# Kernel optimization log

Measured on AMD Instinct MI355X. Metric: run time of the kernel, lower is better.

Reference implementation:

```python
import jax, jax.numpy as jnp
import numpy as np

D_MODEL = 768
N_HEADS = 12
D_K = D_MODEL // N_HEADS
NEG_INF = -1e10


def setup_inputs() -> dict:
    key = jax.random.key(0)
    ks = jax.random.split(key, 12)
    B, S = 2, 4096
    scale = 1.0 / np.sqrt(D_MODEL)
    inp = {
        "q": jax.random.normal(ks[0], (B, S, D_MODEL), jnp.float32),
        "k": jax.random.normal(ks[1], (B, S, D_MODEL), jnp.float32),
        "v": jax.random.normal(ks[2], (B, S, D_MODEL), jnp.float32),
        "mask": jnp.ones((B, S), jnp.int32),
        "Wq": jax.random.normal(ks[3], (D_MODEL, D_MODEL), jnp.float32) * scale,
        "bq": jnp.zeros((D_MODEL,), jnp.float32),
        "Wk": jax.random.normal(ks[4], (D_MODEL, D_MODEL), jnp.float32) * scale,
        "bk": jnp.zeros((D_MODEL,), jnp.float32),
        "Wv": jax.random.normal(ks[5], (D_MODEL, D_MODEL), jnp.float32) * scale,
        "bv": jnp.zeros((D_MODEL,), jnp.float32),
        "Wo": jax.random.normal(ks[6], (D_MODEL, D_MODEL), jnp.float32) * scale,
        "bo": jnp.zeros((D_MODEL,), jnp.float32),
    }
    return inp


def reference(q, k, v, mask, Wq, bq, Wk, bk, Wv, bv, Wo, bo):
    B, Sq, _ = q.shape
    Sk = k.shape[1]
    # linear projections (flax Linear: x @ kernel + bias)
    query = q @ Wq + bq
    key_ = k @ Wk + bk
    value = v @ Wv + bv
    # split heads: [B, H, S, d_k]
    query = query.reshape(B, Sq, N_HEADS, D_K).transpose(0, 2, 1, 3)
    key_ = key_.reshape(B, Sk, N_HEADS, D_K).transpose(0, 2, 1, 3)
    value = value.reshape(B, Sk, N_HEADS, D_K).transpose(0, 2, 1, 3)
    # scores [B, H, Sq, Sk]
    scores = jnp.einsum('bhqd,bhkd->bhqk', query, key_) / jnp.sqrt(
        jnp.asarray(D_K, query.dtype))
    m = mask[:, None, None, :]  # 2D mask -> [B,1,1,Sk]
    scores = jnp.where(m == 0, NEG_INF, scores)
    attn = jax.nn.softmax(scores, axis=-1)
    # dropout deterministic (is_training=False): identity
    x = jnp.einsum('bhqk,bhkd->bhqd', attn, value)
    x = x.transpose(0, 2, 1, 3).reshape(B, Sq, D_MODEL)
    return x @ Wo + bo
```

## Files before the change

kernel.cpp:

```cpp
#include <hip/hip_runtime.h>

typedef __attribute__((ext_vector_type(8))) short short8;
typedef __attribute__((ext_vector_type(4))) float floatx4;
typedef __attribute__((ext_vector_type(16))) float floatx16;
typedef unsigned short ushort_t;

#define S_LEN 4096
#define NH 12
#define DK 64
#define DM 768
#define BQ 128
#define LOG2E 1.4426950408889634f

static __device__ __forceinline__ unsigned short f2bf(float f) {
    unsigned int u = __float_as_uint(f);
    u += 0x7FFFu + ((u >> 16) & 1u);
    return (unsigned short)(u >> 16);
}
static __device__ __forceinline__ unsigned pack2(float a, float b) {
    return (unsigned)f2bf(a) | ((unsigned)f2bf(b) << 16);
}
static __device__ __forceinline__ unsigned pack2f(float a, float b) {
    unsigned au = __float_as_uint(a) + 0x8000u;
    unsigned bu = __float_as_uint(b) + 0x8000u;
    return (bu & 0xFFFF0000u) | (au >> 16);
}
static __device__ __forceinline__ void gld_lds16(const void* g, void* l) {
    __builtin_amdgcn_global_load_lds(
        (__attribute__((address_space(1))) void*)g,
        (__attribute__((address_space(3))) void*)l, 16, 0, 0);
}

__global__ __launch_bounds__(256)
void wtrans_kernel(const float* __restrict__ W0, const float* __restrict__ W1,
                   const float* __restrict__ W2, const float* __restrict__ W3,
                   ushort_t* __restrict__ T0, ushort_t* __restrict__ T1,
                   ushort_t* __restrict__ T2, ushort_t* __restrict__ T3) {
    __shared__ float tile[32][33];
    const int z = blockIdx.z;
    const float* W = (z == 0) ? W0 : (z == 1) ? W1 : (z == 2) ? W2 : W3;
    ushort_t* T = (z == 0) ? T0 : (z == 1) ? T1 : (z == 2) ? T2 : T3;
    const int bx = blockIdx.x, by = blockIdx.y;
    const int tx = threadIdx.x, ty = threadIdx.y;
    #pragma unroll
    for (int j = 0; j < 32; j += 8)
        tile[ty + j][tx] = W[(size_t)(by * 32 + ty + j) * DM + bx * 32 + tx];
    __syncthreads();
    #pragma unroll
    for (int j = 0; j < 32; j += 8)
        T[(size_t)(bx * 32 + ty + j) * DM + by * 32 + tx] = f2bf(tile[tx][ty + j]);
}

__global__ __launch_bounds__(256)
void cvt_kernel(const float* __restrict__ A0, const float* __restrict__ A1,
                const float* __restrict__ A2, ushort_t* __restrict__ O0,
                ushort_t* __restrict__ O1, ushort_t* __restrict__ O2) {
    const int z = blockIdx.y;
    const float* A = (z == 0) ? A0 : (z == 1) ? A1 : A2;
    ushort_t* O = (z == 0) ? O0 : (z == 1) ? O1 : O2;
    const size_t i = ((size_t)blockIdx.x * 256 + threadIdx.x) * 8;
    const float4 f0 = *(const float4*)(A + i);
    const float4 f1 = *(const float4*)(A + i + 4);
    uint4 o;
    o.x = pack2(f0.x, f0.y);
    o.y = pack2(f0.z, f0.w);
    o.z = pack2(f1.x, f1.y);
    o.w = pack2(f1.z, f1.w);
    *(uint4*)(O + i) = o;
}

__global__ __launch_bounds__(256)
void vtrans_kernel(const ushort_t* __restrict__ Vn, ushort_t* __restrict__ Vt) {
    __shared__ ushort_t tl[64 * 72];
    const int s0 = blockIdx.x * 64;
    const size_t bh = blockIdx.y;
    const int t = threadIdx.x;
    {
        const int r = t >> 2, c0 = (t & 3) * 16;
        const uint4* src = (const uint4*)(Vn + (bh * S_LEN + s0 + r) * DK + c0);
        uint4 a0 = src[0], a1 = src[1];
        uint4* dst = (uint4*)&tl[r * 72 + c0];
        dst[0] = a0;
        dst[1] = a1;
    }
    __syncthreads();
    {
        const int d = t >> 2, c0 = (t & 3) * 16;
        alignas(16) ushort_t tmp[16];
        #pragma unroll
        for (int j = 0; j < 16; ++j) tmp[j] = tl[(c0 + j) * 72 + d];
        uint4* dst = (uint4*)(Vt + (bh * DK + d) * S_LEN + s0 + c0);
        dst[0] = *(const uint4*)&tmp[0];
        dst[1] = *(const uint4*)&tmp[8];
    }
}

struct GemmArgs {
    const ushort_t* A[3];
    const ushort_t* Wt[3];
    const float* bias[3];
    void* C[3];
    float scale[3];
};

template <int MODE>
__global__ __launch_bounds__(256, 3)
void gemm_kernel(GemmArgs args) {
    __shared__ ushort_t As[128 * 32];
    __shared__ ushort_t Bs[128 * 32];
    const int z = blockIdx.z;
    const ushort_t* A = args.A[z];
    const ushort_t* Wt = args.Wt[z];
    const float* bias = args.bias[z];
    void* Carg = args.C[z];
    const float scale = args.scale[z];

    const int m0 = blockIdx.x * 128;
    const int n0 = blockIdx.y * 128;
    const int t = threadIdx.x;
    const int w = t >> 6, lane = t & 63, l15 = lane & 15, quad = lane >> 4;
    const int rowoff = (w >> 1) * 64, coloff = (w & 1) * 64;
    const int srow = w * 16 + (lane >> 2);
    const int scol = (lane & 3) * 8;

    floatx4 acc[4][4];
    #pragma unroll
    for (int i = 0; i < 4; ++i)
        #pragma unroll
        for (int j = 0; j < 4; ++j) acc[i][j] = (floatx4){0.f, 0.f, 0.f, 0.f};

    for (int kt = 0; kt < DM; kt += 32) {
        __syncthreads();
        #pragma unroll
        for (int j = 0; j < 2; ++j) {
            const int r = j * 64 + srow;
            gld_lds16(A + (size_t)(m0 + r) * DM + kt + scol, &As[r * 32 + scol]);
            gld_lds16(Wt + (size_t)(n0 + r) * DM + kt + scol, &Bs[r * 32 + scol]);
        }
        __asm__ __volatile__("s_waitcnt vmcnt(0)" ::: "memory");
        __syncthreads();
        short8 af[4], bfr[4];
        #pragma unroll
        for (int i = 0; i < 4; ++i)
            af[i] = *(const short8*)&As[(rowoff + 16 * i + l15) * 32 + quad * 8];
        #pragma unroll
        for (int j = 0; j < 4; ++j)
            bfr[j] = *(const short8*)&Bs[(coloff + 16 * j + l15) * 32 + quad * 8];
        #pragma unroll
        for (int i = 0; i < 4; ++i)
            #pragma unroll
            for (int j = 0; j < 4; ++j)
                acc[i][j] = __builtin_amdgcn_mfma_f32_16x16x32_bf16(af[i], bfr[j], acc[i][j], 0, 0, 0);
    }

    #pragma unroll
    for (int i = 0; i < 4; ++i) {
        #pragma unroll
        for (int j = 0; j < 4; ++j) {
            #pragma unroll
            for (int reg = 0; reg < 4; ++reg) {
                const int m = m0 + rowoff + 16 * i + quad * 4 + reg;
                const int n = n0 + coloff + 16 * j + l15;
                const float v2 = (acc[i][j][reg] + bias[n]) * scale;
                if (MODE == 0) {
                    ushort_t* Out = (ushort_t*)Carg;
                    const int b = m >> 12, s = m & 4095, h = n >> 6, d = n & 63;
                    Out[((size_t)((b * NH + h) * S_LEN + s)) * DK + d] = f2bf(v2);
                } else {
                    float* Out = (float*)Carg;
                    Out[(size_t)m * DM + n] = v2;
                }
            }
        }
    }
}

__global__ __launch_bounds__(256, 3)
void attn_kernel(const ushort_t* __restrict__ Q, const ushort_t* __restrict__ K,
                 const ushort_t* __restrict__ VT, const int* __restrict__ mask,
                 ushort_t* __restrict__ X) {
    __shared__ ushort_t Qs[BQ * DK];
    __shared__ ushort_t Ks0[64 * DK], Ks1[64 * DK];
    __shared__ ushort_t Vs0[64 * DK], Vs1[64 * DK];

    const int id = blockIdx.x;
    const int per = id >> 3;
    const int bh = (id & 7) * 3 + (per >> 5);
    const int qb = per & 31;
    const int b = bh / NH, h = bh - b * NH;
    const size_t bho = (size_t)bh * S_LEN;
    const ushort_t* Vbase = VT + (size_t)bh * DK * S_LEN;
    const int t = threadIdx.x;
    const int w = t >> 6, lane = t & 63, l31 = lane & 31, half = lane >> 5;
    const int q0 = qb * BQ;
    const int swl = l31 & 7;
    const int frow8 = lane >> 3;
    const int fcc = lane & 7;

    auto fillK = [&](int kv0, ushort_t* Kb) {
        #pragma unroll
        for (int j = 0; j < 2; ++j) {
            const int r = (w * 2 + j) * 8 + frow8;
            const int c8 = fcc ^ (r & 7);
            gld_lds16(K + (bho + kv0 + r) * DK + c8 * 8, &Kb[r * DK + fcc * 8]);
        }
    };
    auto fillV = [&](int kv0, ushort_t* Vb) {
        #pragma unroll
        for (int j = 0; j < 2; ++j) {
            const int r = (w * 2 + j) * 8 + frow8;
            const int c8 = fcc ^ (r & 7);
            gld_lds16(Vbase + (size_t)r * S_LEN + kv0 + c8 * 8, &Vb[r * DK + fcc * 8]);
        }
    };

    fillK(0, Ks0);
    fillV(0, Vs0);
    #pragma unroll
    for (int j = 0; j < 4; ++j) {
        const int r = (w * 4 + j) * 8 + frow8;
        const int c8 = fcc ^ (r & 7);
        gld_lds16(Q + (bho + q0 + r) * DK + c8 * 8, &Qs[r * DK + fcc * 8]);
    }
    int ok = 1;
    {
        const int* mrow = mask + (size_t)b * S_LEN + t * 16;
        #pragma unroll
        for (int i = 0; i < 4; ++i) {
            const int4 mm = *(const int4*)(mrow + i * 4);
            ok &= (mm.x != 0) & (mm.y != 0) & (mm.z != 0) & (mm.w != 0);
        }
    }
    const int allones = __syncthreads_and(ok);

    short8 qf[4];
    #pragma unroll
    for (int ks = 0; ks < 4; ++ks) {
        const int c8 = ks * 2 + half;
        qf[ks] = *(const short8*)&Qs[(w * 32 + l31) * DK + ((c8 ^ swl) << 3)];
    }
    ushort_t* Ps = &Qs[(w * 32) * DK];

    floatx16 o[2];
    #pragma unroll
    for (int dt = 0; dt < 2; ++dt)
        #pragma unroll
        for (int r = 0; r < 16; ++r) o[dt][r] = 0.f;
    float l_r = 0.f;

    auto body = [&](int it, const ushort_t* Kc, const ushort_t* Vc,
                    ushort_t* Kn, ushort_t* Vn) {
        __syncthreads();
        if (it + 1 < S_LEN / 64) {
            fillK((it + 1) * 64, Kn);
            fillV((it + 1) * 64, Vn);
        }
        unsigned long long mb = ~0ULL;
        if (!allones) {
            const int mv = mask[(size_t)b * S_LEN + it * 64 + lane];
            mb = __ballot(mv != 0);
        }

        floatx16 st[2];
        #pragma unroll
        for (int kt = 0; kt < 2; ++kt) {
            floatx16 s;
            #pragma unroll
            for (int r = 0; r < 16; ++r) s[r] = 0.f;
            #pragma unroll
            for (int ks = 0; ks < 4; ++ks) {
                const int c8 = ks * 2 + half;
                const short8 kf = *(const short8*)&Kc[(kt * 32 + l31) * DK + ((c8 ^ swl) << 3)];
                s = __builtin_amdgcn_mfma_f32_32x32x16_bf16(kf, qf[ks], s, 0, 0, 0);
            }
            st[kt] = s;
        }

        if (mb != ~0ULL) {
            #pragma unroll
            for (int kt = 0; kt < 2; ++kt) {
                const unsigned bits = (unsigned)(mb >> (kt * 32));
                const unsigned vbits = bits >> (half * 4);
                #pragma unroll
                for (int r = 0; r < 16; ++r)
                    if (!((vbits >> ((r & 3) + 8 * (r >> 2))) & 1)) st[kt][r] = -3.0e10f;
            }
        }

        #pragma unroll
        for (int kt = 0; kt < 2; ++kt) {
            #pragma unroll
            for (int g = 0; g < 4; ++g) {
                const float p0 = __builtin_amdgcn_exp2f(st[kt][g * 4 + 0]);
                const float p1 = __builtin_amdgcn_exp2f(st[kt][g * 4 + 1]);
                const float p2 = __builtin_amdgcn_exp2f(st[kt][g * 4 + 2]);
                const float p3 = __builtin_amdgcn_exp2f(st[kt][g * 4 + 3]);
                l_r += (p0 + p1) + (p2 + p3);
                const int c8 = kt * 4 + g;
                uint2 pk;
                pk.x = pack2f(p0, p1);
                pk.y = pack2f(p2, p3);
                *(uint2*)&Ps[l31 * DK + ((c8 ^ swl) << 3) + half * 4] = pk;
            }
        }
        __asm__ __volatile__("" ::: "memory");

        short8 pf[4];
        #pragma unroll
        for (int ks = 0; ks < 4; ++ks) {
            const int c8 = ks * 2 + half;
            pf[ks] = *(const short8*)&Ps[l31 * DK + ((c8 ^ swl) << 3)];
        }
        #pragma unroll
        for (int dt = 0; dt < 2; ++dt) {
            #pragma unroll
            for (int ks = 0; ks < 4; ++ks) {
                const int c8 = ks * 2 + half;
                const short8 vf = *(const short8*)&Vc[(dt * 32 + l31) * DK + ((c8 ^ swl) << 3)];
                o[dt] = __builtin_amdgcn_mfma_f32_32x32x16_bf16(pf[ks], vf, o[dt], 0, 0, 0);
            }
        }
    };

    for (int it = 0; it < S_LEN / 64; it += 2) {
        body(it, Ks0, Vs0, Ks1, Vs1);
        body(it + 1, Ks1, Vs1, Ks0, Vs0);
    }

    l_r += __shfl_xor(l_r, 32);
    const float inv = 1.0f / l_r;
    float iv[16];
    #pragma unroll
    for (int r = 0; r < 16; ++r)
        iv[r] = __shfl(inv, (r & 3) + 8 * (r >> 2) + 4 * half);
    #pragma unroll
    for (int dt = 0; dt < 2; ++dt)
        #pragma unroll
        for (int r = 0; r < 16; ++r) {
            const int qrow = (r & 3) + 8 * (r >> 2) + 4 * half;
            const int s = q0 + w * 32 + qrow;
            const int d = h * DK + dt * 32 + l31;
            X[((size_t)b * S_LEN + s) * DM + d] = f2bf(o[dt][r] * iv[r]);
        }
}

extern "C" void kernel_launch(void* const* d_in, const int* in_sizes, int n_in,
                              void* d_out, int out_size, void* d_ws, size_t ws_size,
                              hipStream_t stream) {
    const float* q = (const float*)d_in[0];
    const float* k = (const float*)d_in[1];
    const float* v = (const float*)d_in[2];
    const int* mask = (const int*)d_in[3];
    const float* Wq = (const float*)d_in[4];
    const float* bq = (const float*)d_in[5];
    const float* Wk = (const float*)d_in[6];
    const float* bk = (const float*)d_in[7];
    const float* Wv = (const float*)d_in[8];
    const float* bv = (const float*)d_in[9];
    const float* Wo = (const float*)d_in[10];
    const float* bo = (const float*)d_in[11];
    float* out = (float*)d_out;

    const size_t ME = (size_t)2 * S_LEN * DM;
    const size_t WE = (size_t)DM * DM;
    ushort_t* Qb = (ushort_t*)d_ws;
    ushort_t* Kb = Qb + ME;
    ushort_t* Vb = Kb + ME;
    ushort_t* VTb = Vb + ME;
    ushort_t* Xb = VTb + ME;
    ushort_t* Wqt = Xb + ME;
    ushort_t* Wkt = Wqt + WE;
    ushort_t* Wvt = Wkt + WE;
    ushort_t* Wot = Wvt + WE;
    ushort_t* Qa = Xb;
    ushort_t* Ka = VTb;
    ushort_t* Va = (ushort_t*)d_out;

    wtrans_kernel<<<dim3(DM / 32, DM / 32, 4), dim3(32, 8), 0, stream>>>(
        Wq, Wk, Wv, Wo, Wqt, Wkt, Wvt, Wot);

    cvt_kernel<<<dim3((int)(ME / 8 / 256), 3), 256, 0, stream>>>(q, k, v, Qa, Ka, Va);

    GemmArgs g1;
    g1.A[0] = Qa;  g1.A[1] = Ka;  g1.A[2] = Va;
    g1.Wt[0] = Wqt; g1.Wt[1] = Wkt; g1.Wt[2] = Wvt;
    g1.bias[0] = bq; g1.bias[1] = bk; g1.bias[2] = bv;
    g1.C[0] = Qb;  g1.C[1] = Kb;  g1.C[2] = Vb;
    g1.scale[0] = 0.125f * LOG2E;
    g1.scale[1] = 1.0f; g1.scale[2] = 1.0f;
    gemm_kernel<0><<<dim3((2 * S_LEN) / 128, DM / 128, 3), 256, 0, stream>>>(g1);

    vtrans_kernel<<<dim3(S_LEN / 64, 2 * NH), 256, 0, stream>>>(Vb, VTb);

    attn_kernel<<<dim3(768), 256, 0, stream>>>(Qb, Kb, VTb, mask, Xb);

    GemmArgs g2;
    g2.A[0] = Xb;  g2.A[1] = Xb;  g2.A[2] = Xb;
    g2.Wt[0] = Wot; g2.Wt[1] = Wot; g2.Wt[2] = Wot;
    g2.bias[0] = bo; g2.bias[1] = bo; g2.bias[2] = bo;
    g2.C[0] = out; g2.C[1] = out; g2.C[2] = out;
    g2.scale[0] = 1.0f; g2.scale[1] = 1.0f; g2.scale[2] = 1.0f;
    gemm_kernel<1><<<dim3((2 * S_LEN) / 128, DM / 128, 1), 256, 0, stream>>>(g2);
}
```

Before: 348.4 us.

## Keep softmax probabilities in registers by permuting K rows and swapping MFMA operands

K rows are loaded into LDS in a permuted order. As a result, the score accumulator layout from the QK^T MFMA already matches the B-operand layout needed for the PV MFMA, with V taken as the A operand. This removes the LDS round-trip for the P tile and lets the output be written as packed 4-element stores per row instead of scattered 2-byte stores with shuffles. Separately, the weight-transpose and fp32-to-bf16 conversion kernels are merged into one launch. The main risk is a mismatch between the permuted layout and the mask bit mapping.

```diff
diff --git a/kernel.cpp b/kernel.cpp
--- a/kernel.cpp
+++ b/kernel.cpp
@@ -30,43 +30,47 @@
         (__attribute__((address_space(1))) void*)g,
         (__attribute__((address_space(3))) void*)l, 16, 0, 0);
 }
+union U4S8 { uint4 u; short8 s; };
 
 __global__ __launch_bounds__(256)
-void wtrans_kernel(const float* __restrict__ W0, const float* __restrict__ W1,
-                   const float* __restrict__ W2, const float* __restrict__ W3,
-                   ushort_t* __restrict__ T0, ushort_t* __restrict__ T1,
-                   ushort_t* __restrict__ T2, ushort_t* __restrict__ T3) {
-    __shared__ float tile[32][33];
-    const int z = blockIdx.z;
-    const float* W = (z == 0) ? W0 : (z == 1) ? W1 : (z == 2) ? W2 : W3;
-    ushort_t* T = (z == 0) ? T0 : (z == 1) ? T1 : (z == 2) ? T2 : T3;
-    const int bx = blockIdx.x, by = blockIdx.y;
-    const int tx = threadIdx.x, ty = threadIdx.y;
-    #pragma unroll
-    for (int j = 0; j < 32; j += 8)
-        tile[ty + j][tx] = W[(size_t)(by * 32 + ty + j) * DM + bx * 32 + tx];
-    __syncthreads();
-    #pragma unroll
-    for (int j = 0; j < 32; j += 8)
-        T[(size_t)(bx * 32 + ty + j) * DM + by * 32 + tx] = f2bf(tile[tx][ty + j]);
-}
-
-__global__ __launch_bounds__(256)
-void cvt_kernel(const float* __restrict__ A0, const float* __restrict__ A1,
-                const float* __restrict__ A2, ushort_t* __restrict__ O0,
-                ushort_t* __restrict__ O1, ushort_t* __restrict__ O2) {
-    const int z = blockIdx.y;
-    const float* A = (z == 0) ? A0 : (z == 1) ? A1 : A2;
-    ushort_t* O = (z == 0) ? O0 : (z == 1) ? O1 : O2;
-    const size_t i = ((size_t)blockIdx.x * 256 + threadIdx.x) * 8;
-    const float4 f0 = *(const float4*)(A + i);
-    const float4 f1 = *(const float4*)(A + i + 4);
-    uint4 o;
-    o.x = pack2(f0.x, f0.y);
-    o.y = pack2(f0.z, f0.w);
-    o.z = pack2(f1.x, f1.y);
-    o.w = pack2(f1.z, f1.w);
-    *(uint4*)(O + i) = o;
+void prep_kernel(const float* __restrict__ W0, const float* __restrict__ W1,
+                 const float* __restrict__ W2, const float* __restrict__ W3,
+                 ushort_t* __restrict__ T0, ushort_t* __restrict__ T1,
+                 ushort_t* __restrict__ T2, ushort_t* __restrict__ T3,
+                 const float* __restrict__ A0, const float* __restrict__ A1,
+                 const float* __restrict__ A2, ushort_t* __restrict__ O0,
+                 ushort_t* __restrict__ O1, ushort_t* __restrict__ O2) {
+    const int bid = blockIdx.x;
+    const int t = threadIdx.x;
+    if (bid < 2304) {
+        __shared__ float tile[32][33];
+        const int z = bid / 576, rem = bid % 576;
+        const int by = rem / 24, bx = rem % 24;
+        const float* W = (z == 0) ? W0 : (z == 1) ? W1 : (z == 2) ? W2 : W3;
+        ushort_t* T = (z == 0) ? T0 : (z == 1) ? T1 : (z == 2) ? T2 : T3;
+        const int tx = t & 31, ty = t >> 5;
+        #pragma unroll
+        for (int j = 0; j < 32; j += 8)
+            tile[ty + j][tx] = W[(size_t)(by * 32 + ty + j) * DM + bx * 32 + tx];
+        __syncthreads();
+        #pragma unroll
+        for (int j = 0; j < 32; j += 8)
+            T[(size_t)(bx * 32 + ty + j) * DM + by * 32 + tx] = f2bf(tile[tx][ty + j]);
+    } else {
+        const int c = bid - 2304;
+        const int z = c / 3072, blk = c % 3072;
+        const float* A = (z == 0) ? A0 : (z == 1) ? A1 : A2;
+        ushort_t* O = (z == 0) ? O0 : (z == 1) ? O1 : O2;
+        const size_t i = ((size_t)blk * 256 + t) * 8;
+        const float4 f0 = *(const float4*)(A + i);
+        const float4 f1 = *(const float4*)(A + i + 4);
+        uint4 o;
+        o.x = pack2(f0.x, f0.y);
+        o.y = pack2(f0.z, f0.w);
+        o.z = pack2(f1.x, f1.y);
+        o.w = pack2(f1.z, f1.w);
+        *(uint4*)(O + i) = o;
+    }
 }
 
 __global__ __launch_bounds__(256)
@@ -197,12 +201,15 @@
     const int frow8 = lane >> 3;
     const int fcc = lane & 7;
 
+    auto sigma = [](int r) { return (r & ~12) | ((r & 4) << 1) | ((r & 8) >> 1); };
+
     auto fillK = [&](int kv0, ushort_t* Kb) {
         #pragma unroll
         for (int j = 0; j < 2; ++j) {
             const int r = (w * 2 + j) * 8 + frow8;
+            const int gr = sigma(r);
             const int c8 = fcc ^ (r & 7);
-            gld_lds16(K + (bho + kv0 + r) * DK + c8 * 8, &Kb[r * DK + fcc * 8]);
+            gld_lds16(K + (bho + kv0 + gr) * DK + c8 * 8, &Kb[r * DK + fcc * 8]);
         }
     };
     auto fillV = [&](int kv0, ushort_t* Vb) {
@@ -239,7 +246,6 @@
         const int c8 = ks * 2 + half;
         qf[ks] = *(const short8*)&Qs[(w * 32 + l31) * DK + ((c8 ^ swl) << 3)];
     }
-    ushort_t* Ps = &Qs[(w * 32) * DK];
 
     floatx16 o[2];
     #pragma unroll
@@ -278,46 +284,44 @@
 
         if (mb != ~0ULL) {
             #pragma unroll
-            for (int kt = 0; kt < 2; ++kt) {
-                const unsigned bits = (unsigned)(mb >> (kt * 32));
-                const unsigned vbits = bits >> (half * 4);
+            for (int kt = 0; kt < 2; ++kt)
                 #pragma unroll
-                for (int r = 0; r < 16; ++r)
-                    if (!((vbits >> ((r & 3) + 8 * (r >> 2))) & 1)) st[kt][r] = -3.0e10f;
-            }
-        }
-
+                for (int reg = 0; reg < 16; ++reg) {
+                    const int kv = 32 * kt + 8 * half + (reg & 3) +
+                                   4 * ((reg >> 2) & 1) + 16 * (reg >> 3);
+                    if (!((mb >> kv) & 1)) st[kt][reg] = -3.0e10f;
+                }
+        }
+
+        short8 pf[4];
         #pragma unroll
         for (int kt = 0; kt < 2; ++kt) {
-            #pragma unroll
-            for (int g = 0; g < 4; ++g) {
-                const float p0 = __builtin_amdgcn_exp2f(st[kt][g * 4 + 0]);
-                const float p1 = __builtin_amdgcn_exp2f(st[kt][g * 4 + 1]);
-                const float p2 = __builtin_amdgcn_exp2f(st[kt][g * 4 + 2]);
-                const float p3 = __builtin_amdgcn_exp2f(st[kt][g * 4 + 3]);
-                l_r += (p0 + p1) + (p2 + p3);
-                const int c8 = kt * 4 + g;
-                uint2 pk;
-                pk.x = pack2f(p0, p1);
-                pk.y = pack2f(p2, p3);
-                *(uint2*)&Ps[l31 * DK + ((c8 ^ swl) << 3) + half * 4] = pk;
-            }
-        }
-        __asm__ __volatile__("" ::: "memory");
-
-        short8 pf[4];
-        #pragma unroll
-        for (int ks = 0; ks < 4; ++ks) {
-            const int c8 = ks * 2 + half;
-            pf[ks] = *(const short8*)&Ps[l31 * DK + ((c8 ^ swl) << 3)];
-        }
+            floatx16 p;
+            #pragma unroll
+            for (int r = 0; r < 16; ++r) p[r] = __builtin_amdgcn_exp2f(st[kt][r]);
+            #pragma unroll
+            for (int r = 0; r < 16; r += 4)
+                l_r += (p[r] + p[r + 1]) + (p[r + 2] + p[r + 3]);
+            U4S8 u0, u1;
+            u0.u.x = pack2f(p[0], p[1]);
+            u0.u.y = pack2f(p[2], p[3]);
+            u0.u.z = pack2f(p[4], p[5]);
+            u0.u.w = pack2f(p[6], p[7]);
+            u1.u.x = pack2f(p[8], p[9]);
+            u1.u.y = pack2f(p[10], p[11]);
+            u1.u.z = pack2f(p[12], p[13]);
+            u1.u.w = pack2f(p[14], p[15]);
+            pf[2 * kt + 0] = u0.s;
+            pf[2 * kt + 1] = u1.s;
+        }
+
         #pragma unroll
         for (int dt = 0; dt < 2; ++dt) {
             #pragma unroll
             for (int ks = 0; ks < 4; ++ks) {
                 const int c8 = ks * 2 + half;
                 const short8 vf = *(const short8*)&Vc[(dt * 32 + l31) * DK + ((c8 ^ swl) << 3)];
-                o[dt] = __builtin_amdgcn_mfma_f32_32x32x16_bf16(pf[ks], vf, o[dt], 0, 0, 0);
+                o[dt] = __builtin_amdgcn_mfma_f32_32x32x16_bf16(vf, pf[ks], o[dt], 0, 0, 0);
             }
         }
     };
@@ -329,18 +333,20 @@
 
     l_r += __shfl_xor(l_r, 32);
     const float inv = 1.0f / l_r;
-    float iv[16];
-    #pragma unroll
-    for (int r = 0; r < 16; ++r)
-        iv[r] = __shfl(inv, (r & 3) + 8 * (r >> 2) + 4 * half);
+    const int s = q0 + w * 32 + l31;
+    ushort_t* Xrow = X + ((size_t)b * S_LEN + s) * DM + h * DK;
     #pragma unroll
     for (int dt = 0; dt < 2; ++dt)
         #pragma unroll
-        for (int r = 0; r < 16; ++r) {
-            const int qrow = (r & 3) + 8 * (r >> 2) + 4 * half;
-            const int s = q0 + w * 32 + qrow;
-            const int d = h * DK + dt * 32 + l31;
-            X[((size_t)b * S_LEN + s) * DM + d] = f2bf(o[dt][r] * iv[r]);
+        for (int g = 0; g < 4; ++g) {
+            const float a0 = o[dt][4 * g + 0] * inv;
+            const float a1 = o[dt][4 * g + 1] * inv;
+            const float a2 = o[dt][4 * g + 2] * inv;
+            const float a3 = o[dt][4 * g + 3] * inv;
+            uint2 pk;
+            pk.x = pack2(a0, a1);
+            pk.y = pack2(a2, a3);
+            *(uint2*)&Xrow[dt * 32 + 8 * g + 4 * half] = pk;
         }
 }
 
@@ -376,10 +382,8 @@
     ushort_t* Ka = VTb;
     ushort_t* Va = (ushort_t*)d_out;
 
-    wtrans_kernel<<<dim3(DM / 32, DM / 32, 4), dim3(32, 8), 0, stream>>>(
-        Wq, Wk, Wv, Wo, Wqt, Wkt, Wvt, Wot);
-
-    cvt_kernel<<<dim3((int)(ME / 8 / 256), 3), 256, 0, stream>>>(q, k, v, Qa, Ka, Va);
+    prep_kernel<<<dim3(2304 + 9216), 256, 0, stream>>>(
+        Wq, Wk, Wv, Wo, Wqt, Wkt, Wvt, Wot, q, k, v, Qa, Ka, Va);
 
     GemmArgs g1;
     g1.A[0] = Qa;  g1.A[1] = Ka;  g1.A[2] = Va;
```

Measured after the change: 396.5 us. +13.8%, slower.
